# Kernel optimization log

Hardware: AMD Instinct MI355X
Metric: run time of the kernel (lower is better)

## Reference

```python
import jax, jax.numpy as jnp
import numpy as np

N_NODES = 50000
N_EDGES = 200000
D_FEAT = 364
D_OUT = 150
N_PAIRS = 8192
NEG_SLOPE = 0.01
EPS = 1e-12


def setup_inputs() -> dict:
    key = jax.random.key(0)
    ks = jax.random.split(key, 12)
    features = jax.random.normal(ks[0], (N_NODES, D_FEAT), dtype=jnp.float32)
    src = jax.random.randint(ks[1], (N_EDGES,), 0, N_NODES)
    dst = jax.random.randint(ks[2], (N_EDGES,), 0, N_NODES)
    v1 = jax.random.randint(ks[3], (N_PAIRS,), 0, N_NODES)
    v2 = jax.random.randint(ks[4], (N_PAIRS,), 0, N_NODES)
    s = 1.0 / np.sqrt(D_FEAT)
    W1 = jax.random.normal(ks[5], (D_FEAT, D_FEAT), dtype=jnp.float32) * s
    b1 = jax.random.normal(ks[6], (D_FEAT,), dtype=jnp.float32) * s
    W2 = jax.random.normal(ks[7], (D_FEAT, D_FEAT), dtype=jnp.float32) * s
    b2 = jax.random.normal(ks[8], (D_FEAT,), dtype=jnp.float32) * s
    W3 = jax.random.normal(ks[9], (D_FEAT, D_OUT), dtype=jnp.float32) * s
    b3 = jax.random.normal(ks[10], (D_OUT,), dtype=jnp.float32) * s
    return {"features": features, "src": src, "dst": dst, "v1": v1, "v2": v2,
            "W1": W1, "b1": b1, "W2": W2, "b2": b2, "W3": W3, "b3": b3}


def _gcn_sum_layer(x, src, dst, W, b):
    # DGL copy_u/sum: each dst node sums src features over incoming edges.
    agg = jax.ops.segment_sum(x[src], dst, num_segments=N_NODES)  # [N, D]
    h = agg + x  # residual
    return h @ W + b


def _l2_normalize(x):
    norm = jnp.sqrt(jnp.sum(x * x, axis=1, keepdims=True))
    return x / jnp.maximum(norm, EPS)


def reference(features, src, dst, v1, v2, W1, b1, W2, b2, W3, b3):
    lrelu = lambda x: jax.nn.leaky_relu(x, negative_slope=NEG_SLOPE)
    gcn = lrelu(_gcn_sum_layer(features, src, dst, W1, b1))
    gcn = lrelu(_gcn_sum_layer(gcn, src, dst, W2, b2))
    z1 = _l2_normalize(lrelu(gcn[v1] @ W3 + b3))
    z2 = _l2_normalize(lrelu(gcn[v2] @ W3 + b3))
    return (z1, z2)
```

## Files before the change

kernel.cpp:

```cpp
#include <hip/hip_runtime.h>

#define NN 50000
#define NE 200000
#define DF 364
#define KP 384
#define DOUT 150
#define NP 8192
#define NEG_SLOPE 0.01f

typedef float f32x4 __attribute__((ext_vector_type(4)));
typedef short bf16x8 __attribute__((ext_vector_type(8)));
typedef unsigned short u16x8 __attribute__((ext_vector_type(8)));

__device__ __forceinline__ unsigned short f2bf(float x) {
    unsigned u = __float_as_uint(x);
    u += 0x7FFF + ((u >> 16) & 1);
    return (unsigned short)(u >> 16);
}
__device__ __forceinline__ float bf2f(unsigned short h) {
    return __uint_as_float(((unsigned)h) << 16);
}

__device__ __forceinline__ void mfma16(f32x4& d, bf16x8 a, bf16x8 b) {
    d = __builtin_amdgcn_mfma_f32_16x16x32_bf16(a, b, d, 0, 0, 0);
}



__global__ void hist_kernel(const int* __restrict__ dst, int* __restrict__ deg, int n) {
    int t = blockIdx.x * blockDim.x + threadIdx.x;
    if (t < n) atomicAdd(&deg[dst[t]], 1);
}

__global__ __launch_bounds__(1024) void scan_block(const int* __restrict__ deg,
                                                   int* __restrict__ rowptr,
                                                   int* __restrict__ bsum, int n) {
    __shared__ int lds[1024];
    int b = blockIdx.x, t = threadIdx.x;
    int i = b * 1024 + t;
    int v = (i < n) ? deg[i] : 0;
    lds[t] = v;
    __syncthreads();
    for (int off = 1; off < 1024; off <<= 1) {
        int x = (t >= off) ? lds[t - off] : 0;
        __syncthreads();
        lds[t] += x;
        __syncthreads();
    }
    if (i < n) rowptr[i] = lds[t] - v;
    if (t == 1023) bsum[b] = lds[1023];
}

__global__ void scan_small(int* __restrict__ bsum, int nb) {
    int t = threadIdx.x;
    int orig = (t < nb) ? bsum[t] : 0;
    int v = orig;
#pragma unroll
    for (int off = 1; off < 64; off <<= 1) {
        int u = __shfl_up(v, off, 64);
        if (t >= off) v += u;
    }
    if (t < nb) bsum[t] = v - orig;
}

__global__ __launch_bounds__(1024) void add_off(int* __restrict__ rowptr,
                                                const int* __restrict__ bsum,
                                                int* __restrict__ pos, int n) {
    int i = blockIdx.x * 1024 + threadIdx.x;
    if (i < n) {
        int v = rowptr[i] + bsum[blockIdx.x];
        rowptr[i] = v;
        pos[i] = v;
    }
}

__global__ void fill_kernel(const int* __restrict__ src, const int* __restrict__ dst,
                            int* __restrict__ pos, int* __restrict__ esrc, int n) {
    int t = blockIdx.x * blockDim.x + threadIdx.x;
    if (t < n) {
        int j = atomicAdd(&pos[dst[t]], 1);
        esrc[j] = src[t];
    }
}


__device__ __forceinline__ ushort4 round4(float4 v) {
    ushort4 h;
    h.x = f2bf(v.x); h.y = f2bf(v.y); h.z = f2bf(v.z); h.w = f2bf(v.w);
    return h;
}

__device__ __forceinline__ float4 bf4tof4(ushort4 u) {
    return make_float4(bf2f(u.x), bf2f(u.y), bf2f(u.z), bf2f(u.w));
}

__device__ __forceinline__ void f4add(float4& a, const float4 b) {
    a.x += b.x; a.y += b.y; a.z += b.z; a.w += b.w;
}

__device__ __forceinline__ size_t frag_off_lo(int g, int rr, int i) {
    return (size_t)(g * 12 + (i >> 3)) * 512 + ((i >> 1) & 3) * 128 + rr * 8 + (i & 1) * 4;
}
__device__ __forceinline__ size_t frag_off_hi(int g, int rr, int i) {
    return (size_t)(g * 12 + 8 + (i >> 3)) * 512 + ((i >> 1) & 3) * 128 + rr * 8 + (i & 1) * 4;
}


__global__ __launch_bounds__(256) void feat2bf(const float* __restrict__ x,
                                               ushort* __restrict__ o, int n4) {
    int i = blockIdx.x * 256 + threadIdx.x;
    if (i < n4) {
        float4 v = *(const float4*)&x[(size_t)i * 4];
        *(ushort4*)&o[(size_t)i * 4] = round4(v);
    }
}


__global__ __launch_bounds__(256) void agg1_kernel(
    const ushort* __restrict__ xb, const int* __restrict__ rowptr,
    const int* __restrict__ deg, const int* __restrict__ esrc,
    ushort* __restrict__ of, int nrows) {
    int wid = (blockIdx.x * 256 + threadIdx.x) >> 6;
    if (wid >= nrows) return;
    int lane = threadIdx.x & 63;
    int start = rowptr[wid];
    int d = deg[wid];
    bool hi2 = lane < 27;

    const ushort* xr = xb + (size_t)wid * DF;
    float4 a0 = bf4tof4(*(const ushort4*)&xr[4 * lane]);
    float4 a1 = hi2 ? bf4tof4(*(const ushort4*)&xr[256 + 4 * lane])
                    : make_float4(0.f, 0.f, 0.f, 0.f);

    int j = 0;
    for (; j + 1 < d; j += 2) {
        int s0 = esrc[start + j], s1 = esrc[start + j + 1];
        const ushort* r0 = xb + (size_t)s0 * DF;
        const ushort* r1 = xb + (size_t)s1 * DF;
        ushort4 b0 = *(const ushort4*)&r0[4 * lane];
        ushort4 b1 = *(const ushort4*)&r1[4 * lane];
        f4add(a0, bf4tof4(b0));
        f4add(a0, bf4tof4(b1));
        if (hi2) {
            ushort4 c0 = *(const ushort4*)&r0[256 + 4 * lane];
            ushort4 c1 = *(const ushort4*)&r1[256 + 4 * lane];
            f4add(a1, bf4tof4(c0));
            f4add(a1, bf4tof4(c1));
        }
    }
    if (j < d) {
        int s0 = esrc[start + j];
        const ushort* r0 = xb + (size_t)s0 * DF;
        f4add(a0, bf4tof4(*(const ushort4*)&r0[4 * lane]));
        if (hi2) f4add(a1, bf4tof4(*(const ushort4*)&r0[256 + 4 * lane]));
    }

    int g = wid >> 4, rr = wid & 15;
    *(ushort4*)&of[frag_off_lo(g, rr, lane)] = round4(a0);
    if (lane < 32) {
        float4 v = hi2 ? a1 : make_float4(0.f, 0.f, 0.f, 0.f);
        *(ushort4*)&of[frag_off_hi(g, rr, lane)] = round4(v);
    }
}


__global__ __launch_bounds__(256) void agg2_kernel(
    const ushort* __restrict__ h1, const int* __restrict__ rowptr,
    const int* __restrict__ deg, const int* __restrict__ esrc,
    const int* __restrict__ v1, const int* __restrict__ v2,
    ushort* __restrict__ of, int nrows) {
    int wid = (blockIdx.x * 256 + threadIdx.x) >> 6;
    if (wid >= nrows) return;
    int lane = threadIdx.x & 63;
    int node = (wid < NP) ? v1[wid] : v2[wid - NP];
    int start = rowptr[node];
    int d = deg[node];
    bool act = lane < 48;

    float f[8] = {};
    if (act) {
        u16x8 v = *(const u16x8*)&h1[(size_t)node * KP + lane * 8];
#pragma unroll
        for (int i = 0; i < 8; ++i) f[i] = bf2f(v[i]);
    }
    for (int j = 0; j < d; ++j) {
        int s = esrc[start + j];
        if (act) {
            u16x8 v = *(const u16x8*)&h1[(size_t)s * KP + lane * 8];
#pragma unroll
            for (int i = 0; i < 8; ++i) f[i] += bf2f(v[i]);
        }
    }
    if (act) {
        u16x8 o;
#pragma unroll
        for (int i = 0; i < 8; ++i) o[i] = f2bf(f[i]);
        int g = wid >> 4, rr = wid & 15;
        size_t off = (size_t)(g * 12 + (lane >> 2)) * 512 + (lane & 3) * 128 + rr * 8;
        *(u16x8*)&of[off] = o;
    }
}


__global__ void prep_w(const float* __restrict__ W, int K, int Nn,
                       ushort* __restrict__ th, ushort* __restrict__ tl) {
    int idx = blockIdx.x * 256 + threadIdx.x;
    if (idx >= KP * KP) return;
    int e = idx & 7;
    int rr = (idx >> 3) & 15;
    int sub = (idx >> 7) & 3;
    int gc = idx >> 9;
    int g = gc / 12, c = gc - g * 12;
    int k = c * 32 + sub * 8 + e;
    int n = g * 16 + rr;
    float v = (k < K && n < Nn) ? W[(size_t)k * Nn + n] : 0.f;
    unsigned short h = f2bf(v);
    th[idx] = h;
    tl[idx] = f2bf(v - bf2f(h));
}


__global__ __launch_bounds__(256, 3) void gemm_lds(
    const ushort* __restrict__ Awh, const ushort* __restrict__ Awl,
    const ushort* __restrict__ Bact, const float* __restrict__ bias,
    ushort* __restrict__ Cbf, float* __restrict__ Cf32,
    int Nrow, int mode) {
    __shared__ __align__(16) ushort lds[2][3][4096];

    int tid = threadIdx.x;
    int lane = tid & 63;
    int wv = tid >> 6;
    int wr = wv >> 1, wc = wv & 1;
    int brow = blockIdx.x * 128, bcol = blockIdx.y * 128;
    int rg = brow >> 4, cg = bcol >> 4;

#define STAGE(buf, tt)                                                                  \
    do {                                                                                \
        _Pragma("unroll") for (int j_ = 0; j_ < 6; ++j_) {                              \
            int g24_ = wv * 6 + j_;                                                     \
            int p_ = g24_ >> 3, gg_ = g24_ & 7;                                         \
            const ushort* base_ = (p_ == 0) ? Awh : ((p_ == 1) ? Awl : Bact);           \
            int grp_ = ((p_ == 2) ? cg : rg) + gg_;                                     \
            const ushort* s_ = base_ + ((size_t)grp_ * 12 + (tt)) * 512 + lane * 8;     \
            __builtin_amdgcn_global_load_lds(                                           \
                (const __attribute__((address_space(1))) unsigned int*)s_,              \
                (__attribute__((address_space(3))) unsigned int*)(&lds[buf][p_][gg_ * 512]), \
                16, 0, 0);                                                              \
        }                                                                               \
    } while (0)

    int flo = (lane >> 4) * 128 + (lane & 15) * 8;

    f32x4 acc[4][4];
#pragma unroll
    for (int m = 0; m < 4; ++m)
#pragma unroll
        for (int n = 0; n < 4; ++n) acc[m][n] = (f32x4){0.f, 0.f, 0.f, 0.f};

    STAGE(0, 0);
    __syncthreads();

    for (int t = 0; t < KP / 32; ++t) {
        int cur = t & 1;
        if (t + 1 < KP / 32) STAGE(1 - cur, t + 1);
        bf16x8 ah[4], al[4], b[4];
#pragma unroll
        for (int m = 0; m < 4; ++m) {
            ah[m] = *(const bf16x8*)&lds[cur][0][(wr * 4 + m) * 512 + flo];
            al[m] = *(const bf16x8*)&lds[cur][1][(wr * 4 + m) * 512 + flo];
        }
#pragma unroll
        for (int n = 0; n < 4; ++n)
            b[n] = *(const bf16x8*)&lds[cur][2][(wc * 4 + n) * 512 + flo];
#pragma unroll
        for (int m = 0; m < 4; ++m)
#pragma unroll
            for (int n = 0; n < 4; ++n) {
                mfma16(acc[m][n], ah[m], b[n]);
                mfma16(acc[m][n], al[m], b[n]);
            }
        __syncthreads();
    }
#undef STAGE

    int crow_l = (lane >> 4) * 4;
    int ccol_l = lane & 15;
#pragma unroll
    for (int m = 0; m < 4; ++m) {
        int rb = brow + wr * 64 + m * 16 + crow_l;
        float bq[4];
        if (rb + 3 < Nrow) {
            float4 t = *(const float4*)&bias[rb];
            bq[0] = t.x; bq[1] = t.y; bq[2] = t.z; bq[3] = t.w;
        } else {
#pragma unroll
            for (int r = 0; r < 4; ++r) bq[r] = (rb + r < Nrow) ? bias[rb + r] : 0.f;
        }
#pragma unroll
        for (int n = 0; n < 4; ++n) {
            int col = bcol + wc * 64 + n * 16 + ccol_l;
            float v[4];
#pragma unroll
            for (int r = 0; r < 4; ++r) {
                float x = acc[m][n][r] + bq[r];
                v[r] = (x >= 0.f) ? x : NEG_SLOPE * x;
            }
            if (mode == 0) {
                ushort4 h;
                h.x = f2bf(v[0]); h.y = f2bf(v[1]); h.z = f2bf(v[2]); h.w = f2bf(v[3]);
                *(ushort4*)&Cbf[(size_t)col * KP + rb] = h;
            } else if (mode == 1) {
                ushort4 h;
                h.x = f2bf(v[0]); h.y = f2bf(v[1]); h.z = f2bf(v[2]); h.w = f2bf(v[3]);
                size_t off = ((size_t)(col >> 4) * 12 + (rb >> 5)) * 512 +
                             ((rb >> 3) & 3) * 128 + (col & 15) * 8 + (rb & 7);
                *(ushort4*)&Cbf[off] = h;
            } else {
                float* op = Cf32 + (size_t)col * DOUT + rb;
                if (rb + 3 < Nrow) {
                    *(float2*)op = make_float2(v[0], v[1]);
                    *(float2*)(op + 2) = make_float2(v[2], v[3]);
                } else {
#pragma unroll
                    for (int r = 0; r < 4; ++r)
                        if (rb + r < Nrow) op[r] = v[r];
                }
            }
        }
    }
}


__global__ __launch_bounds__(256) void norm_kernel(float* __restrict__ out, int nrows) {
    int wid = (blockIdx.x * 256 + threadIdx.x) >> 6;
    if (wid >= nrows) return;
    int lane = threadIdx.x & 63;
    float* row = out + (size_t)wid * DOUT;
    float a = row[lane];
    float b = row[lane + 64];
    float cc = (lane + 128 < DOUT) ? row[lane + 128] : 0.f;
    float s = a * a + b * b + cc * cc;
#pragma unroll
    for (int off = 32; off; off >>= 1) s += __shfl_xor(s, off, 64);
    float scale = 1.0f / fmaxf(sqrtf(s), 1e-12f);
    row[lane] = a * scale;
    row[lane + 64] = b * scale;
    if (lane + 128 < DOUT) row[lane + 128] = cc * scale;
}


extern "C" void kernel_launch(void* const* d_in, const int* in_sizes, int n_in,
                              void* d_out, int out_size, void* d_ws, size_t ws_size,
                              hipStream_t stream) {
    const float* features = (const float*)d_in[0];
    const int* src = (const int*)d_in[1];
    const int* dst = (const int*)d_in[2];
    const int* v1 = (const int*)d_in[3];
    const int* v2 = (const int*)d_in[4];
    const float* W1 = (const float*)d_in[5];
    const float* b1 = (const float*)d_in[6];
    const float* W2 = (const float*)d_in[7];
    const float* b2 = (const float*)d_in[8];
    const float* W3 = (const float*)d_in[9];
    const float* b3 = (const float*)d_in[10];
    float* out = (float*)d_out;

    const int MPAD = 50048;
    const size_t PLANE = (size_t)MPAD * KP;
    const size_t WSZ = (size_t)KP * KP;

    char* p = (char*)d_ws;
    ushort* a1f = (ushort*)p; p += PLANE * 2;
    ushort* h1 = (ushort*)p; p += PLANE * 2;
    ushort* fbf = (ushort*)p; p += (size_t)NN * DF * 2;
    ushort* wt1h = (ushort*)p; p += WSZ * 2;
    ushort* wt1l = (ushort*)p; p += WSZ * 2;
    ushort* wt2h = (ushort*)p; p += WSZ * 2;
    ushort* wt2l = (ushort*)p; p += WSZ * 2;
    ushort* wt3h = (ushort*)p; p += WSZ * 2;
    ushort* wt3l = (ushort*)p; p += WSZ * 2;
    int* deg = (int*)p; p += NN * 4;
    int* rowptr = (int*)p; p += NN * 4;
    int* pos = (int*)p; p += NN * 4;
    int* esrc = (int*)p; p += NE * 4;
    int* bsum = (int*)p; p += 256;
    ushort* a2f = a1f;
    ushort* h2t = h1;

    const int NSB = (NN + 1023) / 1024;

    hipMemsetAsync(deg, 0, NN * sizeof(int), stream);
    hist_kernel<<<(NE + 255) / 256, 256, 0, stream>>>(dst, deg, NE);
    scan_block<<<NSB, 1024, 0, stream>>>(deg, rowptr, bsum, NN);
    scan_small<<<1, 64, 0, stream>>>(bsum, NSB);
    add_off<<<NSB, 1024, 0, stream>>>(rowptr, bsum, pos, NN);
    fill_kernel<<<(NE + 255) / 256, 256, 0, stream>>>(src, dst, pos, esrc, NE);

    feat2bf<<<(NN * DF / 4 + 255) / 256, 256, 0, stream>>>(features, fbf, NN * DF / 4);
    prep_w<<<(KP * KP + 255) / 256, 256, 0, stream>>>(W1, DF, DF, wt1h, wt1l);
    prep_w<<<(KP * KP + 255) / 256, 256, 0, stream>>>(W2, DF, DF, wt2h, wt2l);
    prep_w<<<(KP * KP + 255) / 256, 256, 0, stream>>>(W3, DF, DOUT, wt3h, wt3l);

    agg1_kernel<<<(NN * 64 + 255) / 256, 256, 0, stream>>>(fbf, rowptr, deg, esrc,
                                                           a1f, NN);
    gemm_lds<<<dim3(3, 391), 256, 0, stream>>>(wt1h, wt1l, a1f, b1,
                                               h1, nullptr, DF, 0);

    const int NR = 2 * NP;
    agg2_kernel<<<(NR * 64 + 255) / 256, 256, 0, stream>>>(h1, rowptr, deg, esrc,
                                                           v1, v2, a2f, NR);
    gemm_lds<<<dim3(3, 128), 256, 0, stream>>>(wt2h, wt2l, a2f, b2,
                                               h2t, nullptr, DF, 1);

    gemm_lds<<<dim3(2, 128), 256, 0, stream>>>(wt3h, wt3l, h2t, b3,
                                               nullptr, out, DOUT, 2);
    norm_kernel<<<(NR * 64 + 255) / 256, 256, 0, stream>>>(out, NR);
}
```

Measured before the change: 302.7 us.

## Drop low-order weight split in first two GEMMs and fuse prep kernels

The first two GEMMs now use only the bf16 high part of the weights, dropping the hi/lo split-precision correction. This halves their MFMA count and the weight traffic staged into LDS. The histogram, feature cast and weight prep kernels are also merged into one launch. The cost is lower accuracy in layers 1 and 2, while the output layer keeps the split.

```diff
diff --git a/kernel.cpp b/kernel.cpp
--- a/kernel.cpp
+++ b/kernel.cpp
@@ -26,11 +26,6 @@
 }
 
 
-
-__global__ void hist_kernel(const int* __restrict__ dst, int* __restrict__ deg, int n) {
-    int t = blockIdx.x * blockDim.x + threadIdx.x;
-    if (t < n) atomicAdd(&deg[dst[t]], 1);
-}
 
 __global__ __launch_bounds__(1024) void scan_block(const int* __restrict__ deg,
                                                    int* __restrict__ rowptr,
@@ -106,12 +101,49 @@
 }
 
 
-__global__ __launch_bounds__(256) void feat2bf(const float* __restrict__ x,
-                                               ushort* __restrict__ o, int n4) {
-    int i = blockIdx.x * 256 + threadIdx.x;
-    if (i < n4) {
-        float4 v = *(const float4*)&x[(size_t)i * 4];
-        *(ushort4*)&o[(size_t)i * 4] = round4(v);
+#define NBF 17774
+#define NW 576
+#define NH 782
+
+__device__ __forceinline__ void prep_w_one(const float* __restrict__ W, int K, int Nn,
+                                           ushort* __restrict__ th, ushort* __restrict__ tl,
+                                           int idx) {
+    if (idx >= KP * KP) return;
+    int e = idx & 7;
+    int rr = (idx >> 3) & 15;
+    int sub = (idx >> 7) & 3;
+    int gc = idx >> 9;
+    int g = gc / 12, c = gc - g * 12;
+    int k = c * 32 + sub * 8 + e;
+    int n = g * 16 + rr;
+    float v = (k < K && n < Nn) ? W[(size_t)k * Nn + n] : 0.f;
+    unsigned short h = f2bf(v);
+    th[idx] = h;
+    if (tl) tl[idx] = f2bf(v - bf2f(h));
+}
+
+__global__ __launch_bounds__(256) void prep_all(
+    const float* __restrict__ features, ushort* __restrict__ fbf,
+    const float* __restrict__ W1, ushort* __restrict__ wt1,
+    const float* __restrict__ W2, ushort* __restrict__ wt2,
+    const float* __restrict__ W3, ushort* __restrict__ wt3h, ushort* __restrict__ wt3l,
+    const int* __restrict__ dst, int* __restrict__ deg) {
+    int b = blockIdx.x, tid = threadIdx.x;
+    if (b < NBF) {
+        int i = b * 256 + tid;
+        if (i < NN * DF / 4) {
+            float4 v = *(const float4*)&features[(size_t)i * 4];
+            *(ushort4*)&fbf[(size_t)i * 4] = round4(v);
+        }
+    } else if (b < NBF + NW) {
+        prep_w_one(W1, DF, DF, wt1, nullptr, (b - NBF) * 256 + tid);
+    } else if (b < NBF + 2 * NW) {
+        prep_w_one(W2, DF, DF, wt2, nullptr, (b - NBF - NW) * 256 + tid);
+    } else if (b < NBF + 3 * NW) {
+        prep_w_one(W3, DF, DOUT, wt3h, wt3l, (b - NBF - 2 * NW) * 256 + tid);
+    } else {
+        int t = (b - NBF - 3 * NW) * 256 + tid;
+        if (t < NE) atomicAdd(&deg[dst[t]], 1);
     }
 }
 
@@ -202,30 +234,14 @@
 }
 
 
-__global__ void prep_w(const float* __restrict__ W, int K, int Nn,
-                       ushort* __restrict__ th, ushort* __restrict__ tl) {
-    int idx = blockIdx.x * 256 + threadIdx.x;
-    if (idx >= KP * KP) return;
-    int e = idx & 7;
-    int rr = (idx >> 3) & 15;
-    int sub = (idx >> 7) & 3;
-    int gc = idx >> 9;
-    int g = gc / 12, c = gc - g * 12;
-    int k = c * 32 + sub * 8 + e;
-    int n = g * 16 + rr;
-    float v = (k < K && n < Nn) ? W[(size_t)k * Nn + n] : 0.f;
-    unsigned short h = f2bf(v);
-    th[idx] = h;
-    tl[idx] = f2bf(v - bf2f(h));
-}
-
-
+template <int WP>
 __global__ __launch_bounds__(256, 3) void gemm_lds(
     const ushort* __restrict__ Awh, const ushort* __restrict__ Awl,
     const ushort* __restrict__ Bact, const float* __restrict__ bias,
     ushort* __restrict__ Cbf, float* __restrict__ Cf32,
     int Nrow, int mode) {
-    __shared__ __align__(16) ushort lds[2][3][4096];
+    constexpr int PL = WP + 1;
+    __shared__ __align__(16) ushort lds[2][PL][4096];
 
     int tid = threadIdx.x;
     int lane = tid & 63;
@@ -236,11 +252,11 @@
 
 #define STAGE(buf, tt)                                                                  \
     do {                                                                                \
-        _Pragma("unroll") for (int j_ = 0; j_ < 6; ++j_) {                              \
-            int g24_ = wv * 6 + j_;                                                     \
+        _Pragma("unroll") for (int j_ = 0; j_ < 2 * PL; ++j_) {                         \
+            int g24_ = wv * 2 * PL + j_;                                                \
             int p_ = g24_ >> 3, gg_ = g24_ & 7;                                         \
-            const ushort* base_ = (p_ == 0) ? Awh : ((p_ == 1) ? Awl : Bact);           \
-            int grp_ = ((p_ == 2) ? cg : rg) + gg_;                                     \
+            const ushort* base_ = (p_ == 0) ? Awh : ((WP == 2 && p_ == 1) ? Awl : Bact);\
+            int grp_ = ((p_ == WP) ? cg : rg) + gg_;                                    \
             const ushort* s_ = base_ + ((size_t)grp_ * 12 + (tt)) * 512 + lane * 8;     \
             __builtin_amdgcn_global_load_lds(                                           \
                 (const __attribute__((address_space(1))) unsigned int*)s_,              \
@@ -267,17 +283,17 @@
 #pragma unroll
         for (int m = 0; m < 4; ++m) {
             ah[m] = *(const bf16x8*)&lds[cur][0][(wr * 4 + m) * 512 + flo];
-            al[m] = *(const bf16x8*)&lds[cur][1][(wr * 4 + m) * 512 + flo];
+            if (WP == 2) al[m] = *(const bf16x8*)&lds[cur][1][(wr * 4 + m) * 512 + flo];
         }
 #pragma unroll
         for (int n = 0; n < 4; ++n)
-            b[n] = *(const bf16x8*)&lds[cur][2][(wc * 4 + n) * 512 + flo];
+            b[n] = *(const bf16x8*)&lds[cur][WP][(wc * 4 + n) * 512 + flo];
 #pragma unroll
         for (int m = 0; m < 4; ++m)
 #pragma unroll
             for (int n = 0; n < 4; ++n) {
                 mfma16(acc[m][n], ah[m], b[n]);
-                mfma16(acc[m][n], al[m], b[n]);
+                if (WP == 2) mfma16(acc[m][n], al[m], b[n]);
             }
         __syncthreads();
     }
@@ -373,10 +389,8 @@
     ushort* a1f = (ushort*)p; p += PLANE * 2;
     ushort* h1 = (ushort*)p; p += PLANE * 2;
     ushort* fbf = (ushort*)p; p += (size_t)NN * DF * 2;
-    ushort* wt1h = (ushort*)p; p += WSZ * 2;
-    ushort* wt1l = (ushort*)p; p += WSZ * 2;
-    ushort* wt2h = (ushort*)p; p += WSZ * 2;
-    ushort* wt2l = (ushort*)p; p += WSZ * 2;
+    ushort* wt1 = (ushort*)p; p += WSZ * 2;
+    ushort* wt2 = (ushort*)p; p += WSZ * 2;
     ushort* wt3h = (ushort*)p; p += WSZ * 2;
     ushort* wt3l = (ushort*)p; p += WSZ * 2;
     int* deg = (int*)p; p += NN * 4;
@@ -390,29 +404,25 @@
     const int NSB = (NN + 1023) / 1024;
 
     hipMemsetAsync(deg, 0, NN * sizeof(int), stream);
-    hist_kernel<<<(NE + 255) / 256, 256, 0, stream>>>(dst, deg, NE);
+    prep_all<<<NBF + 3 * NW + NH, 256, 0, stream>>>(features, fbf, W1, wt1, W2, wt2,
+                                                    W3, wt3h, wt3l, dst, deg);
     scan_block<<<NSB, 1024, 0, stream>>>(deg, rowptr, bsum, NN);
     scan_small<<<1, 64, 0, stream>>>(bsum, NSB);
     add_off<<<NSB, 1024, 0, stream>>>(rowptr, bsum, pos, NN);
     fill_kernel<<<(NE + 255) / 256, 256, 0, stream>>>(src, dst, pos, esrc, NE);
 
-    feat2bf<<<(NN * DF / 4 + 255) / 256, 256, 0, stream>>>(features, fbf, NN * DF / 4);
-    prep_w<<<(KP * KP + 255) / 256, 256, 0, stream>>>(W1, DF, DF, wt1h, wt1l);
-    prep_w<<<(KP * KP + 255) / 256, 256, 0, stream>>>(W2, DF, DF, wt2h, wt2l);
-    prep_w<<<(KP * KP + 255) / 256, 256, 0, stream>>>(W3, DF, DOUT, wt3h, wt3l);
-
     agg1_kernel<<<(NN * 64 + 255) / 256, 256, 0, stream>>>(fbf, rowptr, deg, esrc,
                                                            a1f, NN);
-    gemm_lds<<<dim3(3, 391), 256, 0, stream>>>(wt1h, wt1l, a1f, b1,
-                                               h1, nullptr, DF, 0);
+    gemm_lds<1><<<dim3(3, 391), 256, 0, stream>>>(wt1, nullptr, a1f, b1,
+                                                  h1, nullptr, DF, 0);
 
     const int NR = 2 * NP;
     agg2_kernel<<<(NR * 64 + 255) / 256, 256, 0, stream>>>(h1, rowptr, deg, esrc,
                                                            v1, v2, a2f, NR);
-    gemm_lds<<<dim3(3, 128), 256, 0, stream>>>(wt2h, wt2l, a2f, b2,
-                                               h2t, nullptr, DF, 1);
-
-    gemm_lds<<<dim3(2, 128), 256, 0, stream>>>(wt3h, wt3l, h2t, b3,
-                                               nullptr, out, DOUT, 2);
+    gemm_lds<1><<<dim3(3, 128), 256, 0, stream>>>(wt2, nullptr, a2f, b2,
+                                                  h2t, nullptr, DF, 1);
+
+    gemm_lds<2><<<dim3(2, 128), 256, 0, stream>>>(wt3h, wt3l, h2t, b3,
+                                                  nullptr, out, DOUT, 2);
     norm_kernel<<<(NR * 64 + 255) / 256, 256, 0, stream>>>(out, NR);
 }
```

New measurement: 289.4 us. -4.4%, faster.
